# Performance work log

Measured on AMD Instinct MI355X. Metric: run time of the kernel, lower is better.

Reference implementation:

```python
import jax, jax.numpy as jnp
import numpy as np

EMBED_DIM = 1024
NUM_HEADS = 16
HEAD_DIM = EMBED_DIM // NUM_HEADS
SCALE = HEAD_DIM ** (-0.5)


def setup_inputs() -> dict:
    key = jax.random.key(0)
    ks = jax.random.split(key, 8)
    B, Nq, Nkv, C = 2, 2048, 2048, EMBED_DIM
    s = C ** (-0.5)
    return {
        "q": jax.random.normal(ks[0], (B, Nq, C), dtype=jnp.float32),
        "kv": jax.random.normal(ks[1], (B, Nkv, C), dtype=jnp.float32),
        "w_q": jax.random.normal(ks[2], (C, C), dtype=jnp.float32) * s,
        "b_q": jnp.zeros((C,), dtype=jnp.float32),
        "w_kv": jax.random.normal(ks[3], (C, 2 * C), dtype=jnp.float32) * s,
        "b_kv": jnp.zeros((2 * C,), dtype=jnp.float32),
        "w_out": jax.random.normal(ks[4], (C, C), dtype=jnp.float32) * s,
        "b_out": jnp.zeros((C,), dtype=jnp.float32),
    }


def reference(q, kv, w_q, b_q, w_kv, b_kv, w_out, b_out):
    B, Nq, C = q.shape
    _, Nkv, _ = kv.shape
    H, D = NUM_HEADS, HEAD_DIM

    # q projection: (B, Nq, C) -> (B, H, Nq, D)
    qp = (q @ w_q + b_q).reshape(B, Nq, H, D).transpose(0, 2, 1, 3)

    # kv projection: (B, Nkv, 2C) -> (2, B, H, Nkv, D); '(two h d)' layout
    kvp = (kv @ w_kv + b_kv).reshape(B, Nkv, 2, H, D).transpose(2, 0, 3, 1, 4)
    kp, vp = kvp[0], kvp[1]

    # attention scores (B, H, Nq, Nkv), softmax over kv axis
    attn = jnp.einsum("bhqd,bhkd->bhqk", qp, kp) * SCALE
    attn = jax.nn.softmax(attn, axis=-1)

    out = jnp.einsum("bhqk,bhkd->bhqd", attn, vp)
    out = out.transpose(0, 2, 1, 3).reshape(B, Nq, C)
    return out @ w_out + b_out
```

## Files before the change

kernel.cpp:

```cpp
#include <hip/hip_runtime.h>

#define NUM_HEADS 16
#define HEAD_DIM 64
#define EMBED 1024

typedef __attribute__((ext_vector_type(8))) short short8;
typedef __attribute__((ext_vector_type(4))) short short4v;
typedef __attribute__((ext_vector_type(4))) float f32x4;

#if __has_builtin(__builtin_amdgcn_exp2f)
#define EXP2F(x) __builtin_amdgcn_exp2f(x)
#else
#define EXP2F(x) exp2f(x)
#endif

__device__ __forceinline__ f32x4 mfma16_bf16(short4v a, short4v b, f32x4 c) {
#if defined(__HIP_DEVICE_COMPILE__)
  return __builtin_amdgcn_mfma_f32_16x16x16bf16_1k(a, b, c, 0, 0, 0);
#else
  return c;
#endif
}

__device__ __forceinline__ unsigned pk_trunc(float x1, float x0) {
#if defined(__HIP_DEVICE_COMPILE__)
  return __builtin_amdgcn_perm(__builtin_bit_cast(unsigned, x1),
                               __builtin_bit_cast(unsigned, x0), 0x07060302u);
#else
  return 0;
#endif
}

__device__ __forceinline__ short f2bf(float f) {
  unsigned u = __builtin_bit_cast(unsigned, f);
  u += 0x7fffu + ((u >> 16) & 1u);
  return (short)(u >> 16);
}

__device__ __forceinline__ void gload_lds16(const void* g, void* l) {
  __builtin_amdgcn_global_load_lds(
      (const __attribute__((address_space(1))) void*)g,
      (__attribute__((address_space(3))) void*)l,
      16, 0, 0);
}

__device__ __forceinline__ void tr_body(const float* __restrict__ in,
                                        short* __restrict__ out, int R, int C,
                                        int bx, int by, float (*t)[33], int tid) {
  int tx = tid & 31, ty = tid >> 5;
#pragma unroll
  for (int i = 0; i < 32; i += 8)
    t[ty + i][tx] = in[(size_t)(by + ty + i) * C + bx + tx];
  __syncthreads();
#pragma unroll
  for (int i = 0; i < 32; i += 8)
    out[(size_t)(bx + ty + i) * R + by + tx] = f2bf(t[tx][ty + i]);
}

__global__ void prep(const float* __restrict__ w_q, short* __restrict__ wqt,
                     const float* __restrict__ w_kv, short* __restrict__ wkvt,
                     const float* __restrict__ w_out, short* __restrict__ wot) {
  __shared__ float t[32][33];
  int bid = blockIdx.x, tid = threadIdx.x;
  if (bid < 1024) {
    tr_body(w_q, wqt, 1024, 1024, (bid & 31) * 32, (bid >> 5) * 32, t, tid);
  } else if (bid < 3072) {
    int r = bid - 1024;
    tr_body(w_kv, wkvt, 1024, 2048, (r & 63) * 32, (r >> 6) * 32, t, tid);
  } else {
    int r = bid - 3072;
    tr_body(w_out, wot, 1024, 1024, (r & 31) * 32, (r >> 5) * 32, t, tid);
  }
}

template <int MODE, bool AF32>
__device__ __forceinline__ void gemm_body(void* Astage, short* Bs,
                                          const void* __restrict__ Aptr,
                                          const short* __restrict__ Bt,
                                          const float* __restrict__ bias,
                                          void* __restrict__ Cptr, int N, int K,
                                          int m0, int n0, float scale) {
  const int tid = threadIdx.x;
  const int wave = tid >> 6, lane = tid & 63;
  const int quad = lane >> 4, l16 = lane & 15;
  const int wr = wave >> 1, wc = wave & 1;

  f32x4 acc[4][4];
#pragma unroll
  for (int i = 0; i < 4; i++)
#pragma unroll
    for (int j = 0; j < 4; j++) acc[i][j] = (f32x4)0.f;

  const int rgrp = lane >> 2;
  const int kecol = (lane & 3) * 8;
  const int rA = lane >> 3;
  const int cA = (lane & 7) ^ (rA & 7);

  for (int k0 = 0; k0 < K; k0 += 32) {
    __syncthreads();
    if (AF32) {
      const float* Af = (const float*)Aptr;
#pragma unroll
      for (int s = 0; s < 4; s++)
        gload_lds16(Af + (size_t)(m0 + wave * 32 + s * 8 + rA) * K + k0 + cA * 4,
                    (char*)Astage + wave * 4096 + s * 1024);
    } else {
      const short* Ab = (const short*)Aptr;
#pragma unroll
      for (int s = 0; s < 2; s++)
        gload_lds16(Ab + (size_t)(m0 + wave * 32 + s * 16 + rgrp) * K + k0 + kecol,
                    (char*)Astage + wave * 2048 + s * 1024);
    }
#pragma unroll
    for (int s = 0; s < 2; s++)
      gload_lds16(Bt + (size_t)(n0 + wave * 32 + s * 16 + rgrp) * K + k0 + kecol,
                  (char*)Bs + wave * 2048 + s * 1024);
    __syncthreads();

    short8 a[4], b[4];
#pragma unroll
    for (int i = 0; i < 4; i++) {
      int row = wr * 64 + i * 16 + l16;
      if (AF32) {
        const float* Asf = (const float*)Astage;
        int ch0 = (2 * quad) ^ (row & 7);
        int ch1 = (2 * quad + 1) ^ (row & 7);
        f32x4 x = *(const f32x4*)(Asf + row * 32 + ch0 * 4);
        f32x4 y = *(const f32x4*)(Asf + row * 32 + ch1 * 4);
        unsigned p0 = pk_trunc(x[1], x[0]);
        unsigned p1 = pk_trunc(x[3], x[2]);
        unsigned p2 = pk_trunc(y[1], y[0]);
        unsigned p3 = pk_trunc(y[3], y[2]);
        uint4 packed = {p0, p1, p2, p3};
        a[i] = __builtin_bit_cast(short8, packed);
      } else {
        a[i] = *(const short8*)((const short*)Astage + row * 32 + quad * 8);
      }
    }
#pragma unroll
    for (int j = 0; j < 4; j++)
      b[j] = *(const short8*)(Bs + (wc * 64 + j * 16 + l16) * 32 + quad * 8);
#pragma unroll
    for (int i = 0; i < 4; i++)
#pragma unroll
      for (int j = 0; j < 4; j++)
        acc[i][j] = __builtin_amdgcn_mfma_f32_16x16x32_bf16(a[i], b[j], acc[i][j], 0, 0, 0);
  }

#pragma unroll
  for (int j = 0; j < 4; j++) {
    int col = n0 + wc * 64 + j * 16 + l16;
    float bv = bias[col];
    if (MODE == 2) {
      int vcol = col - 1024;
      int h = vcol >> 6, d = vcol & 63;
#pragma unroll
      for (int i = 0; i < 4; i++) {
        int rbase = m0 + wr * 64 + i * 16 + quad * 4;
        int b = rbase >> 11;
        int kvr = rbase & 2047;
        short pk[4];
#pragma unroll
        for (int r = 0; r < 4; r++) pk[r] = f2bf(acc[i][j][r] + bv);
        *(uint2*)((short*)Cptr + ((size_t)(b * 16 + h) * 64 + d) * 2048 + kvr) =
            *(uint2*)pk;
      }
    } else {
#pragma unroll
      for (int i = 0; i < 4; i++) {
        int rbase = m0 + wr * 64 + i * 16 + quad * 4;
#pragma unroll
        for (int r = 0; r < 4; r++) {
          float v = (acc[i][j][r] + bv) * scale;
          if (MODE == 1)
            ((float*)Cptr)[(size_t)(rbase + r) * N + col] = v;
          else
            ((short*)Cptr)[(size_t)(rbase + r) * N + col] = f2bf(v);
        }
      }
    }
  }
}

__global__ __launch_bounds__(256)
void gemm_qkv(const float* __restrict__ q, const float* __restrict__ kv,
              const short* __restrict__ wqt, const short* __restrict__ wkvt,
              const float* __restrict__ b_q, const float* __restrict__ b_kv,
              short* __restrict__ qp, short* __restrict__ kvp,
              short* __restrict__ vt) {
  __shared__ float Asf[128 * 32];
  __shared__ short Bs[128 * 32];
  int y = blockIdx.y;
  int m0 = blockIdx.x * 128;
  if (y < 8) {
    gemm_body<0, true>(Asf, Bs, q, wqt, b_q, qp, 1024, 1024, m0, y * 128, 0.125f);
  } else if (y < 16) {
    gemm_body<0, true>(Asf, Bs, kv, wkvt, b_kv, kvp, 2048, 1024, m0, (y - 8) * 128, 1.f);
  } else {
    gemm_body<2, true>(Asf, Bs, kv, wkvt, b_kv, vt, 2048, 1024, m0, (y - 8) * 128, 1.f);
  }
}

__global__ __launch_bounds__(256)
void gemm_out(const short* __restrict__ A, const short* __restrict__ Bt,
              const float* __restrict__ bias, float* __restrict__ C) {
  __shared__ short As[128 * 32];
  __shared__ short Bs[128 * 32];
  gemm_body<1, false>(As, Bs, A, Bt, bias, C, 1024, 1024, blockIdx.x * 128,
                      blockIdx.y * 128, 1.f);
}

__global__ __launch_bounds__(256)
void attn8(const short* __restrict__ qp, const short* __restrict__ kvp,
           const short* __restrict__ vt, short* __restrict__ aout,
           int B, int Nq, int Nkv) {
  __shared__ short Ks0[64 * 64], Ks1[64 * 64];
  __shared__ short Vs0[64 * 64], Vs1[64 * 64];

  const int tid = threadIdx.x;
  const int wave = tid >> 6, lane = tid & 63;
  const int quad = lane >> 4, l16 = lane & 15;
  const int bh = blockIdx.y;
  const int b = bh >> 4, h = bh & 15;
  const int q0 = blockIdx.x * 64;
  const int niter = Nkv / 64;

  const int qrow = q0 + wave * 16 + l16;
  const short* qbase = qp + ((size_t)b * Nq + qrow) * EMBED + h * HEAD_DIM;
  short8 aq0 = *(const short8*)(qbase + quad * 8);
  short8 aq1 = *(const short8*)(qbase + 32 + quad * 8);

  const int rl = lane >> 3;
  const int co = (lane & 7) ^ (rl & 7);
  const short* kgbase = kvp + (size_t)b * Nkv * 2048 + h * HEAD_DIM;
  const short* vgbase = vt + (size_t)(b * 16 + h) * 64 * 2048;

  f32x4 acc[4];
#pragma unroll
  for (int nt = 0; nt < 4; nt++) acc[nt] = (f32x4)0.f;
  float lsum = 0.f;

  const int swz_r = quad ^ (l16 & 7);
  const int swz_r4 = (quad + 4) ^ (l16 & 7);

  auto stage = [&](int it, short* Kd, short* Vd) {
    int kv0 = it * 64;
    gload_lds16(kgbase + (size_t)(kv0 + wave * 16 + rl) * 2048 + co * 8,
                Kd + wave * 1024);
    gload_lds16(kgbase + (size_t)(kv0 + wave * 16 + 8 + rl) * 2048 + co * 8,
                Kd + wave * 1024 + 512);
    gload_lds16(vgbase + (size_t)(wave * 16 + rl) * 2048 + kv0 + co * 8,
                Vd + wave * 1024);
    gload_lds16(vgbase + (size_t)(wave * 16 + 8 + rl) * 2048 + kv0 + co * 8,
                Vd + wave * 1024 + 512);
  };

  auto compute = [&](const short* Kt, const short* Vt_) {
    f32x4 s[4];
#pragma unroll
    for (int jt = 0; jt < 4; jt++) s[jt] = (f32x4)0.f;
#pragma unroll
    for (int jt = 0; jt < 4; ++jt) {
      const short* kr = Kt + (jt * 16 + l16) * 64;
      short8 ka0 = *(const short8*)(kr + swz_r * 8);
      short8 ka1 = *(const short8*)(kr + swz_r4 * 8);
      s[jt] = __builtin_amdgcn_mfma_f32_16x16x32_bf16(ka0, aq0, s[jt], 0, 0, 0);
      s[jt] = __builtin_amdgcn_mfma_f32_16x16x32_bf16(ka1, aq1, s[jt], 0, 0, 0);
    }
    short4v pf[4];
#pragma unroll
    for (int jt = 0; jt < 4; ++jt) {
      float e0 = EXP2F(__builtin_fmaf(s[jt][0], 1.44269504f, -17.3123405f));
      float e1 = EXP2F(__builtin_fmaf(s[jt][1], 1.44269504f, -17.3123405f));
      float e2 = EXP2F(__builtin_fmaf(s[jt][2], 1.44269504f, -17.3123405f));
      float e3 = EXP2F(__builtin_fmaf(s[jt][3], 1.44269504f, -17.3123405f));
      lsum += (e0 + e1) + (e2 + e3);
      uint2 pk = {pk_trunc(e1, e0), pk_trunc(e3, e2)};
      pf[jt] = __builtin_bit_cast(short4v, pk);
    }
#pragma unroll
    for (int jt = 0; jt < 4; ++jt) {
      const int chs = ((jt * 2 + (quad >> 1)) ^ (l16 & 7)) * 8 + (quad & 1) * 4;
#pragma unroll
      for (int nt = 0; nt < 4; ++nt) {
        short4v va = *(const short4v*)(Vt_ + (nt * 16 + l16) * 64 + chs);
        acc[nt] = mfma16_bf16(va, pf[jt], acc[nt]);
      }
    }
  };

  stage(0, Ks0, Vs0);
  for (int it = 0; it < niter; it += 2) {
    __syncthreads();
    stage(min(it + 1, niter - 1), Ks1, Vs1);
    compute(Ks0, Vs0);
    __syncthreads();
    stage(min(it + 2, niter - 1), Ks0, Vs0);
    compute(Ks1, Vs1);
  }

  lsum += __shfl_xor(lsum, 16);
  lsum += __shfl_xor(lsum, 32);
  float inv = 1.f / lsum;
  const int qg = q0 + wave * 16 + l16;
  short* obase = aout + ((size_t)b * Nq + qg) * EMBED + h * HEAD_DIM;
#pragma unroll
  for (int nt = 0; nt < 4; ++nt) {
    short pk[4];
#pragma unroll
    for (int r = 0; r < 4; ++r) pk[r] = f2bf(acc[nt][r] * inv);
    *(uint2*)(obase + nt * 16 + quad * 4) = *(uint2*)pk;
  }
}

extern "C" void kernel_launch(void* const* d_in, const int* in_sizes, int n_in,
                              void* d_out, int out_size, void* d_ws, size_t ws_size,
                              hipStream_t stream) {
  const float* q = (const float*)d_in[0];
  const float* kv = (const float*)d_in[1];
  const float* w_q = (const float*)d_in[2];
  const float* b_q = (const float*)d_in[3];
  const float* w_kv = (const float*)d_in[4];
  const float* b_kv = (const float*)d_in[5];
  const float* w_out = (const float*)d_in[6];
  const float* b_out = (const float*)d_in[7];

  const int B = 2, Nq = 2048, Nkv = 2048, C = 1024;
  const int Mq = B * Nq;

  char* ws = (char*)d_ws;
  short* qp = (short*)ws;
  short* kvp = qp + (size_t)Mq * C;
  short* vt = kvp + (size_t)Mq * 2 * C;
  short* aout = vt + (size_t)Mq * C;
  short* wot = aout + (size_t)Mq * C;
  short* wqt = wot + (size_t)C * C;
  short* wkvt = wqt + (size_t)C * C;

  prep<<<4096, 256, 0, stream>>>(w_q, wqt, w_kv, wkvt, w_out, wot);
  gemm_qkv<<<dim3(Mq / 128, 24), 256, 0, stream>>>(q, kv, wqt, wkvt, b_q, b_kv,
                                                   qp, kvp, vt);
  attn8<<<dim3(Nq / 64, B * NUM_HEADS), 256, 0, stream>>>(qp, kvp, vt, aout,
                                                          B, Nq, Nkv);
  gemm_out<<<dim3(Mq / 128, C / 128), 256, 0, stream>>>(aout, wot, b_out,
                                                        (float*)d_out);
}
```

Baseline: 238.3 us.

## Double-buffer LDS tiles in GEMM body to overlap global loads with MFMA

The shared GEMM routine now keeps two LDS buffers for the A and B tiles. It issues the direct-to-LDS loads for the next K step before computing on the current one, and uses explicit vmcnt waits and barriers in place of two __syncthreads per iteration. The aim is to hide global-memory latency behind MFMA work in both the QKV and output projections. In exchange the LDS footprint per block doubles (about 48KB for the fp32-A kernel), which may reduce occupancy, and the hand-counted vmcnt values must match the number of outstanding loads.

```diff
diff --git a/kernel.cpp b/kernel.cpp
--- a/kernel.cpp
+++ b/kernel.cpp
@@ -74,7 +74,7 @@
 }
 
 template <int MODE, bool AF32>
-__device__ __forceinline__ void gemm_body(void* Astage, short* Bs,
+__device__ __forceinline__ void gemm_body(void* Astage, void* Bstage,
                                           const void* __restrict__ Aptr,
                                           const short* __restrict__ Bt,
                                           const float* __restrict__ bias,
@@ -96,33 +96,57 @@
   const int rA = lane >> 3;
   const int cA = (lane & 7) ^ (rA & 7);
 
-  for (int k0 = 0; k0 < K; k0 += 32) {
-    __syncthreads();
+  const int ASZ = AF32 ? 128 * 32 * 4 : 128 * 32 * 2;
+  const int BSZ = 128 * 32 * 2;
+  char* A0 = (char*)Astage;
+  char* B0 = (char*)Bstage;
+
+  auto stage = [&](int k0, int buf) {
+    char* Ad = A0 + buf * ASZ;
+    char* Bd = B0 + buf * BSZ;
     if (AF32) {
       const float* Af = (const float*)Aptr;
 #pragma unroll
       for (int s = 0; s < 4; s++)
         gload_lds16(Af + (size_t)(m0 + wave * 32 + s * 8 + rA) * K + k0 + cA * 4,
-                    (char*)Astage + wave * 4096 + s * 1024);
+                    Ad + wave * 4096 + s * 1024);
     } else {
       const short* Ab = (const short*)Aptr;
 #pragma unroll
       for (int s = 0; s < 2; s++)
         gload_lds16(Ab + (size_t)(m0 + wave * 32 + s * 16 + rgrp) * K + k0 + kecol,
-                    (char*)Astage + wave * 2048 + s * 1024);
+                    Ad + wave * 2048 + s * 1024);
     }
 #pragma unroll
     for (int s = 0; s < 2; s++)
       gload_lds16(Bt + (size_t)(n0 + wave * 32 + s * 16 + rgrp) * K + k0 + kecol,
-                  (char*)Bs + wave * 2048 + s * 1024);
-    __syncthreads();
+                  Bd + wave * 2048 + s * 1024);
+  };
+
+  stage(0, 0);
+  int cur = 0;
+  for (int k0 = 0; k0 < K; k0 += 32) {
+    if (k0 + 32 < K) {
+      stage(k0 + 32, cur ^ 1);
+      if (AF32)
+        asm volatile("s_waitcnt vmcnt(6)" ::: "memory");
+      else
+        asm volatile("s_waitcnt vmcnt(4)" ::: "memory");
+    } else {
+      asm volatile("s_waitcnt vmcnt(0)" ::: "memory");
+    }
+    __builtin_amdgcn_s_barrier();
+    asm volatile("" ::: "memory");
+
+    const char* Ac = A0 + cur * ASZ;
+    const short* Bc = (const short*)(B0 + cur * BSZ);
 
     short8 a[4], b[4];
 #pragma unroll
     for (int i = 0; i < 4; i++) {
       int row = wr * 64 + i * 16 + l16;
       if (AF32) {
-        const float* Asf = (const float*)Astage;
+        const float* Asf = (const float*)Ac;
         int ch0 = (2 * quad) ^ (row & 7);
         int ch1 = (2 * quad + 1) ^ (row & 7);
         f32x4 x = *(const f32x4*)(Asf + row * 32 + ch0 * 4);
@@ -134,17 +158,22 @@
         uint4 packed = {p0, p1, p2, p3};
         a[i] = __builtin_bit_cast(short8, packed);
       } else {
-        a[i] = *(const short8*)((const short*)Astage + row * 32 + quad * 8);
+        a[i] = *(const short8*)((const short*)Ac + row * 32 + quad * 8);
       }
     }
 #pragma unroll
     for (int j = 0; j < 4; j++)
-      b[j] = *(const short8*)(Bs + (wc * 64 + j * 16 + l16) * 32 + quad * 8);
+      b[j] = *(const short8*)(Bc + (wc * 64 + j * 16 + l16) * 32 + quad * 8);
 #pragma unroll
     for (int i = 0; i < 4; i++)
 #pragma unroll
       for (int j = 0; j < 4; j++)
         acc[i][j] = __builtin_amdgcn_mfma_f32_16x16x32_bf16(a[i], b[j], acc[i][j], 0, 0, 0);
+
+    asm volatile("" ::: "memory");
+    __builtin_amdgcn_s_barrier();
+    asm volatile("" ::: "memory");
+    cur ^= 1;
   }
 
 #pragma unroll
@@ -188,8 +217,8 @@
               const float* __restrict__ b_q, const float* __restrict__ b_kv,
               short* __restrict__ qp, short* __restrict__ kvp,
               short* __restrict__ vt) {
-  __shared__ float Asf[128 * 32];
-  __shared__ short Bs[128 * 32];
+  __shared__ float Asf[2 * 128 * 32];
+  __shared__ short Bs[2 * 128 * 32];
   int y = blockIdx.y;
   int m0 = blockIdx.x * 128;
   if (y < 8) {
@@ -204,8 +233,8 @@
 __global__ __launch_bounds__(256)
 void gemm_out(const short* __restrict__ A, const short* __restrict__ Bt,
               const float* __restrict__ bias, float* __restrict__ C) {
-  __shared__ short As[128 * 32];
-  __shared__ short Bs[128 * 32];
+  __shared__ short As[2 * 128 * 32];
+  __shared__ short Bs[2 * 128 * 32];
   gemm_body<1, false>(As, Bs, A, Bt, bias, C, 1024, 1024, blockIdx.x * 128,
                       blockIdx.y * 128, 1.f);
 }
```

Measured after the change: 241.7 us. About the same (+1.4%).

## Pre-convert activations to bf16 and double-buffer GEMM K-tiles with async loads

Applied to the files above, without the earlier changes.

Activations q and kv are converted to bf16 in the prep kernel, which now launches extra blocks for this. The bf16 copies reuse the aout and d_out buffers as scratch, so the GEMMs no longer stage fp32 tiles and convert them inside the inner loop. The GEMM body now uses K-tiles of 64 with two LDS buffers and prefetches two stages ahead, using explicit waitcnt, barriers and setprio around the MFMA block. This should overlap global loads with compute. In exchange it adds an extra pass over the activations in memory, larger LDS use (64KB per block), and launch_bounds that ask for two blocks per CU.

```diff
diff --git a/kernel.cpp b/kernel.cpp
--- a/kernel.cpp
+++ b/kernel.cpp
@@ -59,7 +59,9 @@
 
 __global__ void prep(const float* __restrict__ w_q, short* __restrict__ wqt,
                      const float* __restrict__ w_kv, short* __restrict__ wkvt,
-                     const float* __restrict__ w_out, short* __restrict__ wot) {
+                     const float* __restrict__ w_out, short* __restrict__ wot,
+                     const float* __restrict__ q, const float* __restrict__ kv,
+                     short* __restrict__ qb, short* __restrict__ kvb) {
   __shared__ float t[32][33];
   int bid = blockIdx.x, tid = threadIdx.x;
   if (bid < 1024) {
@@ -67,15 +69,25 @@
   } else if (bid < 3072) {
     int r = bid - 1024;
     tr_body(w_kv, wkvt, 1024, 2048, (r & 63) * 32, (r >> 6) * 32, t, tid);
-  } else {
+  } else if (bid < 4096) {
     int r = bid - 3072;
     tr_body(w_out, wot, 1024, 1024, (r & 31) * 32, (r >> 5) * 32, t, tid);
-  }
-}
-
-template <int MODE, bool AF32>
-__device__ __forceinline__ void gemm_body(void* Astage, short* Bs,
-                                          const void* __restrict__ Aptr,
+  } else {
+    int r = bid - 4096;
+    const float* src = (r < 2048) ? q : kv;
+    short* dst = (r < 2048) ? qb : kvb;
+    size_t base = (size_t)(r & 2047) * 2048 + (size_t)tid * 8;
+    f32x4 x = *(const f32x4*)(src + base);
+    f32x4 y = *(const f32x4*)(src + base + 4);
+    uint4 p = {pk_trunc(x[1], x[0]), pk_trunc(x[3], x[2]),
+               pk_trunc(y[1], y[0]), pk_trunc(y[3], y[2])};
+    *(uint4*)(dst + base) = p;
+  }
+}
+
+template <int MODE>
+__device__ __forceinline__ void gemm_body(short* As, short* Bs,
+                                          const short* __restrict__ A,
                                           const short* __restrict__ Bt,
                                           const float* __restrict__ bias,
                                           void* __restrict__ Cptr, int N, int K,
@@ -91,60 +103,81 @@
 #pragma unroll
     for (int j = 0; j < 4; j++) acc[i][j] = (f32x4)0.f;
 
-  const int rgrp = lane >> 2;
-  const int kecol = (lane & 3) * 8;
-  const int rA = lane >> 3;
-  const int cA = (lane & 7) ^ (rA & 7);
-
-  for (int k0 = 0; k0 < K; k0 += 32) {
-    __syncthreads();
-    if (AF32) {
-      const float* Af = (const float*)Aptr;
-#pragma unroll
-      for (int s = 0; s < 4; s++)
-        gload_lds16(Af + (size_t)(m0 + wave * 32 + s * 8 + rA) * K + k0 + cA * 4,
-                    (char*)Astage + wave * 4096 + s * 1024);
-    } else {
-      const short* Ab = (const short*)Aptr;
-#pragma unroll
-      for (int s = 0; s < 2; s++)
-        gload_lds16(Ab + (size_t)(m0 + wave * 32 + s * 16 + rgrp) * K + k0 + kecol,
-                    (char*)Astage + wave * 2048 + s * 1024);
-    }
-#pragma unroll
-    for (int s = 0; s < 2; s++)
-      gload_lds16(Bt + (size_t)(n0 + wave * 32 + s * 16 + rgrp) * K + k0 + kecol,
-                  (char*)Bs + wave * 2048 + s * 1024);
-    __syncthreads();
-
-    short8 a[4], b[4];
+  const int srow = lane >> 3;
+  const int schk = (lane & 7) ^ (srow & 7);
+  const int ABUF = 128 * 64;
+  const int NT = K >> 6;
+
+  auto stage = [&](int t, int slot) {
+    int k0 = t * 64;
+    short* Ad = As + slot * ABUF;
+    short* Bd = Bs + slot * ABUF;
+#pragma unroll
+    for (int s = 0; s < 4; s++) {
+      gload_lds16(A + (size_t)(m0 + s * 32 + wave * 8 + srow) * K + k0 + schk * 8,
+                  Ad + s * 2048 + wave * 512);
+      gload_lds16(Bt + (size_t)(n0 + s * 32 + wave * 8 + srow) * K + k0 + schk * 8,
+                  Bd + s * 2048 + wave * 512);
+    }
+  };
+
+  stage(0, 0);
+  stage(1, 1);
+  asm volatile("s_waitcnt vmcnt(8)" ::: "memory");
+  __builtin_amdgcn_s_barrier();
+  asm volatile("" ::: "memory");
+
+  for (int t = 0; t < NT; ++t) {
+    const short* Ac = As + (t & 1) * ABUF;
+    const short* Bc = Bs + (t & 1) * ABUF;
+
+    short8 a[4][2], b[4][2];
 #pragma unroll
     for (int i = 0; i < 4; i++) {
       int row = wr * 64 + i * 16 + l16;
-      if (AF32) {
-        const float* Asf = (const float*)Astage;
-        int ch0 = (2 * quad) ^ (row & 7);
-        int ch1 = (2 * quad + 1) ^ (row & 7);
-        f32x4 x = *(const f32x4*)(Asf + row * 32 + ch0 * 4);
-        f32x4 y = *(const f32x4*)(Asf + row * 32 + ch1 * 4);
-        unsigned p0 = pk_trunc(x[1], x[0]);
-        unsigned p1 = pk_trunc(x[3], x[2]);
-        unsigned p2 = pk_trunc(y[1], y[0]);
-        unsigned p3 = pk_trunc(y[3], y[2]);
-        uint4 packed = {p0, p1, p2, p3};
-        a[i] = __builtin_bit_cast(short8, packed);
-      } else {
-        a[i] = *(const short8*)((const short*)Astage + row * 32 + quad * 8);
-      }
-    }
-#pragma unroll
-    for (int j = 0; j < 4; j++)
-      b[j] = *(const short8*)(Bs + (wc * 64 + j * 16 + l16) * 32 + quad * 8);
+#pragma unroll
+      for (int kh = 0; kh < 2; kh++) {
+        int ch = (kh * 4 + quad) ^ (row & 7);
+        a[i][kh] = *(const short8*)(Ac + row * 64 + ch * 8);
+      }
+    }
+#pragma unroll
+    for (int j = 0; j < 4; j++) {
+      int row = wc * 64 + j * 16 + l16;
+#pragma unroll
+      for (int kh = 0; kh < 2; kh++) {
+        int ch = (kh * 4 + quad) ^ (row & 7);
+        b[j][kh] = *(const short8*)(Bc + row * 64 + ch * 8);
+      }
+    }
+    asm volatile("s_waitcnt lgkmcnt(0)" ::: "memory");
+    __builtin_amdgcn_sched_barrier(0);
+    __builtin_amdgcn_s_barrier();
+    asm volatile("" ::: "memory");
+
+    if (t + 2 < NT) stage(t + 2, t & 1);
+
+    __builtin_amdgcn_s_setprio(1);
 #pragma unroll
     for (int i = 0; i < 4; i++)
 #pragma unroll
-      for (int j = 0; j < 4; j++)
-        acc[i][j] = __builtin_amdgcn_mfma_f32_16x16x32_bf16(a[i], b[j], acc[i][j], 0, 0, 0);
+      for (int j = 0; j < 4; j++) {
+        acc[i][j] = __builtin_amdgcn_mfma_f32_16x16x32_bf16(a[i][0], b[j][0],
+                                                            acc[i][j], 0, 0, 0);
+        acc[i][j] = __builtin_amdgcn_mfma_f32_16x16x32_bf16(a[i][1], b[j][1],
+                                                            acc[i][j], 0, 0, 0);
+      }
+    __builtin_amdgcn_s_setprio(0);
+    asm volatile("" ::: "memory");
+
+    if (t + 2 < NT) {
+      asm volatile("s_waitcnt vmcnt(8)" ::: "memory");
+      __builtin_amdgcn_s_barrier();
+    } else if (t + 1 < NT) {
+      asm volatile("s_waitcnt vmcnt(0)" ::: "memory");
+      __builtin_amdgcn_s_barrier();
+    }
+    asm volatile("" ::: "memory");
   }
 
 #pragma unroll
@@ -182,32 +215,32 @@
   }
 }
 
-__global__ __launch_bounds__(256)
-void gemm_qkv(const float* __restrict__ q, const float* __restrict__ kv,
+__global__ __launch_bounds__(256, 2)
+void gemm_qkv(const short* __restrict__ qb, const short* __restrict__ kvb,
               const short* __restrict__ wqt, const short* __restrict__ wkvt,
               const float* __restrict__ b_q, const float* __restrict__ b_kv,
               short* __restrict__ qp, short* __restrict__ kvp,
               short* __restrict__ vt) {
-  __shared__ float Asf[128 * 32];
-  __shared__ short Bs[128 * 32];
+  __shared__ short As[2 * 128 * 64];
+  __shared__ short Bs[2 * 128 * 64];
   int y = blockIdx.y;
   int m0 = blockIdx.x * 128;
   if (y < 8) {
-    gemm_body<0, true>(Asf, Bs, q, wqt, b_q, qp, 1024, 1024, m0, y * 128, 0.125f);
+    gemm_body<0>(As, Bs, qb, wqt, b_q, qp, 1024, 1024, m0, y * 128, 0.125f);
   } else if (y < 16) {
-    gemm_body<0, true>(Asf, Bs, kv, wkvt, b_kv, kvp, 2048, 1024, m0, (y - 8) * 128, 1.f);
+    gemm_body<0>(As, Bs, kvb, wkvt, b_kv, kvp, 2048, 1024, m0, (y - 8) * 128, 1.f);
   } else {
-    gemm_body<2, true>(Asf, Bs, kv, wkvt, b_kv, vt, 2048, 1024, m0, (y - 8) * 128, 1.f);
-  }
-}
-
-__global__ __launch_bounds__(256)
+    gemm_body<2>(As, Bs, kvb, wkvt, b_kv, vt, 2048, 1024, m0, (y - 8) * 128, 1.f);
+  }
+}
+
+__global__ __launch_bounds__(256, 2)
 void gemm_out(const short* __restrict__ A, const short* __restrict__ Bt,
               const float* __restrict__ bias, float* __restrict__ C) {
-  __shared__ short As[128 * 32];
-  __shared__ short Bs[128 * 32];
-  gemm_body<1, false>(As, Bs, A, Bt, bias, C, 1024, 1024, blockIdx.x * 128,
-                      blockIdx.y * 128, 1.f);
+  __shared__ short As[2 * 128 * 64];
+  __shared__ short Bs[2 * 128 * 64];
+  gemm_body<1>(As, Bs, A, Bt, bias, C, 1024, 1024, blockIdx.x * 128,
+               blockIdx.y * 128, 1.f);
 }
 
 __global__ __launch_bounds__(256)
@@ -336,9 +369,11 @@
   short* wot = aout + (size_t)Mq * C;
   short* wqt = wot + (size_t)C * C;
   short* wkvt = wqt + (size_t)C * C;
-
-  prep<<<4096, 256, 0, stream>>>(w_q, wqt, w_kv, wkvt, w_out, wot);
-  gemm_qkv<<<dim3(Mq / 128, 24), 256, 0, stream>>>(q, kv, wqt, wkvt, b_q, b_kv,
+  short* qb = aout;
+  short* kvb = (short*)d_out;
+
+  prep<<<8192, 256, 0, stream>>>(w_q, wqt, w_kv, wkvt, w_out, wot, q, kv, qb, kvb);
+  gemm_qkv<<<dim3(Mq / 128, 24), 256, 0, stream>>>(qb, kvb, wqt, wkvt, b_q, b_kv,
                                                    qp, kvp, vt);
   attn8<<<dim3(Nq / 64, B * NUM_HEADS), 256, 0, stream>>>(qp, kvp, vt, aout,
                                                           B, Nq, Nkv);
```

Result: faster. 208.4 us (-12.6%).
